# Kernel optimization log

Hardware: AMD Instinct MI355X
Metric: run time of the kernel (lower is better)

Reference implementation:

```python
import jax, jax.numpy as jnp
import numpy as np

B, S, H, D, OUT = 4, 2048, 16, 64, 1024


def setup_inputs() -> dict:
    root = jax.random.key(0)
    ks = jax.random.split(root, 7)
    scale = 0.02
    return {
        "query": jax.random.normal(ks[0], (B, S, D), dtype=jnp.float32),
        "key": jax.random.normal(ks[1], (B, S, D), dtype=jnp.float32),
        "value": jax.random.normal(ks[2], (B, S, D), dtype=jnp.float32),
        # per-head projection weights, torch Linear layout [out, in] stacked over heads
        "Wq": jax.random.normal(ks[3], (H, D, D), dtype=jnp.float32) * scale,
        "Wk": jax.random.normal(ks[4], (H, D, D), dtype=jnp.float32) * scale,
        "Wv": jax.random.normal(ks[5], (H, D, D), dtype=jnp.float32) * scale,
        # output projection weight [output_dim, H*D]
        "Wo": jax.random.normal(ks[6], (OUT, H * D), dtype=jnp.float32) * scale,
    }


def reference(query, key, value, Wq, Wk, Wv, Wo):
    b, s, d = query.shape
    h = Wq.shape[0]
    # per-head linear projections (x @ W_h.T), batched over all heads at once
    q = jnp.einsum('bsd,hed->bhse', query, Wq)   # [B,H,S,D]
    k = jnp.einsum('bsd,hed->bhse', key, Wk)
    v = jnp.einsum('bsd,hed->bhse', value, Wv)
    scores = jnp.einsum('bhqe,bhke->bhqk', q, k) / jnp.sqrt(jnp.asarray(d, q.dtype))
    attn = jax.nn.softmax(scores, axis=-1)       # [B,H,S,S]
    o = jnp.einsum('bhqk,bhke->bhqe', attn, v)   # [B,H,S,D]
    # concat heads along feature dim -> [B,S,H*D]
    x = o.transpose(0, 2, 1, 3).reshape(b, s, h * d)
    return x @ Wo.T                               # [B,S,OUT]
```

## Files before the change

kernel.cpp:

```cpp
#include <hip/hip_runtime.h>
#include <hip/hip_bf16.h>
#include <cstdint>


#define QSCALE 0.1803368801111204f

typedef __attribute__((ext_vector_type(8))) short bf16x8;
typedef __attribute__((ext_vector_type(4))) short bf16x4;
typedef __attribute__((ext_vector_type(4))) float f32x4;
typedef __attribute__((ext_vector_type(16))) float f32x16;

typedef __attribute__((address_space(1))) unsigned int g_u32;
typedef __attribute__((address_space(3))) unsigned int l_u32;

__device__ inline unsigned short f2bf(float f) {
    union { float f; unsigned u; } v;
    v.f = f;
    unsigned r = v.u + 0x7fffu + ((v.u >> 16) & 1u);
    return (unsigned short)(r >> 16);
}

__device__ inline unsigned cvt_pk_bf16(float a, float b) {
    unsigned r;
    asm("v_cvt_pk_bf16_f32 %0, %1, %2" : "=v"(r) : "v"(a), "v"(b));
    return r;
}

__device__ inline f32x4 mfma16(bf16x8 a, bf16x8 b, f32x4 c) {
    return __builtin_amdgcn_mfma_f32_16x16x32_bf16(a, b, c, 0, 0, 0);
}
__device__ inline f32x16 mfma32(bf16x8 a, bf16x8 b, f32x16 c) {
    return __builtin_amdgcn_mfma_f32_32x32x16_bf16(a, b, c, 0, 0, 0);
}

__device__ inline float sum16(const f32x16& v) {
    float a0 = v[0] + v[1], a1 = v[2] + v[3], a2 = v[4] + v[5], a3 = v[6] + v[7];
    float a4 = v[8] + v[9], a5 = v[10] + v[11], a6 = v[12] + v[13], a7 = v[14] + v[15];
    float b0 = a0 + a1, b1 = a2 + a3, b2 = a4 + a5, b3 = a6 + a7;
    return (b0 + b1) + (b2 + b3);
}

__global__ __launch_bounds__(256) void conv_bf16(
    const float* __restrict__ q, const float* __restrict__ k, const float* __restrict__ v,
    const float* __restrict__ wq, const float* __restrict__ wk, const float* __restrict__ wv,
    const float* __restrict__ wo,
    unsigned short* __restrict__ qb, unsigned short* __restrict__ kb,
    unsigned short* __restrict__ vb,
    unsigned short* __restrict__ wqb, unsigned short* __restrict__ wkb,
    unsigned short* __restrict__ wvb, unsigned short* __restrict__ wob) {
    const int z = blockIdx.y;
    const float* src; unsigned short* dst; int n;
    switch (z) {
        case 0: src = q;  dst = qb;  n = 524288;  break;
        case 1: src = k;  dst = kb;  n = 524288;  break;
        case 2: src = v;  dst = vb;  n = 524288;  break;
        case 3: src = wq; dst = wqb; n = 65536;   break;
        case 4: src = wk; dst = wkb; n = 65536;   break;
        case 5: src = wv; dst = wvb; n = 65536;   break;
        default: src = wo; dst = wob; n = 1048576; break;
    }
    int i = (blockIdx.x * 256 + threadIdx.x) * 8;
    if (i >= n) return;
    float4 f0 = *reinterpret_cast<const float4*>(src + i);
    float4 f1 = *reinterpret_cast<const float4*>(src + i + 4);
    bf16x8 h;
    h[0] = (short)f2bf(f0.x); h[1] = (short)f2bf(f0.y);
    h[2] = (short)f2bf(f0.z); h[3] = (short)f2bf(f0.w);
    h[4] = (short)f2bf(f1.x); h[5] = (short)f2bf(f1.y);
    h[6] = (short)f2bf(f1.z); h[7] = (short)f2bf(f1.w);
    *reinterpret_cast<bf16x8*>(dst + i) = h;
}

__global__ __launch_bounds__(256) void qkv_proj(
    const unsigned short* __restrict__ qb, const unsigned short* __restrict__ kb,
    const unsigned short* __restrict__ vb,
    const unsigned short* __restrict__ wqb, const unsigned short* __restrict__ wkb,
    const unsigned short* __restrict__ wvb,
    unsigned short* __restrict__ Qp, unsigned short* __restrict__ Kp,
    unsigned short* __restrict__ Vt) {
    const int z = blockIdx.z;
    const unsigned short* X = (z == 0) ? qb : (z == 1) ? kb : vb;
    const unsigned short* W = (z == 0) ? wqb : (z == 1) ? wkb : wvb;
    const int bh = blockIdx.y;
    const int b = bh >> 4, h = bh & 15;
    const int s0 = blockIdx.x * 64;
    const int t = threadIdx.x;
    const int w = t >> 6, l = t & 63, lr = l & 15, lg = l >> 4;

    __shared__ unsigned short Xs[64][72];
    __shared__ unsigned short Ws[64][72];

    {
        const unsigned short* xsrc = X + (size_t)(b * 2048 + s0) * 64;
        const unsigned short* wsrc = W + h * 4096;
#pragma unroll
        for (int i = 0; i < 2; ++i) {
            int idx = t + i * 256;
            int r = idx >> 3, c8 = (idx & 7) * 8;
            *reinterpret_cast<bf16x8*>(&Xs[r][c8]) =
                *reinterpret_cast<const bf16x8*>(xsrc + (size_t)r * 64 + c8);
            *reinterpret_cast<bf16x8*>(&Ws[r][c8]) =
                *reinterpret_cast<const bf16x8*>(wsrc + r * 64 + c8);
        }
    }
    __syncthreads();

    f32x4 acc[4];
#pragma unroll
    for (int nt = 0; nt < 4; ++nt) acc[nt] = f32x4{0.f, 0.f, 0.f, 0.f};
#pragma unroll
    for (int kk = 0; kk < 2; ++kk) {
        bf16x8 a = *reinterpret_cast<const bf16x8*>(&Xs[w * 16 + lr][kk * 32 + lg * 8]);
#pragma unroll
        for (int nt = 0; nt < 4; ++nt) {
            bf16x8 bb = *reinterpret_cast<const bf16x8*>(&Ws[nt * 16 + lr][kk * 32 + lg * 8]);
            acc[nt] = mfma16(a, bb, acc[nt]);
        }
    }

    const size_t bhS = (size_t)bh * 2048 * 64;
    if (z < 2) {
        unsigned short* Out = (z == 0) ? Qp : Kp;
        const float scale = (z == 0) ? QSCALE : 1.0f;
#pragma unroll
        for (int nt = 0; nt < 4; ++nt)
#pragma unroll
            for (int j = 0; j < 4; ++j) {
                int s = s0 + w * 16 + lg * 4 + j;
                int e = nt * 16 + lr;
                Out[bhS + (size_t)s * 64 + e] = f2bf(acc[nt][j] * scale);
            }
    } else {
#pragma unroll
        for (int nt = 0; nt < 4; ++nt) {
            int e = nt * 16 + lr;
            int s = s0 + w * 16 + lg * 4;
            bf16x4 pk;
#pragma unroll
            for (int j = 0; j < 4; ++j) pk[j] = (short)f2bf(acc[nt][j]);
            *reinterpret_cast<bf16x4*>(&Vt[(size_t)bh * 64 * 2048 + (size_t)e * 2048 + s]) = pk;
        }
    }
}

__global__ __launch_bounds__(256) void attn_kernel(
    const unsigned short* __restrict__ Qp, const unsigned short* __restrict__ Kp,
    const unsigned short* __restrict__ Vt, unsigned short* __restrict__ Xb) {
    const int bh = blockIdx.y;
    const int b = bh >> 4, h = bh & 15;
    const int t = threadIdx.x;
    const int w = t >> 6, l = t & 63;
    const int lo = l & 31, hi = l >> 5;
    const int qw = blockIdx.x * 128 + w * 32;

    __shared__ unsigned short Kbuf[2][4096];
    __shared__ unsigned short Vbuf[2][4096];

    bf16x8 bq[4];
    {
        const unsigned short* qptr = Qp + ((size_t)bh * 2048 + qw + lo) * 64 + hi * 8;
#pragma unroll
        for (int ds = 0; ds < 4; ++ds)
            bq[ds] = *reinterpret_cast<const bf16x8*>(qptr + ds * 16);
    }

    f32x16 oacc0, oacc1;
#pragma unroll
    for (int r = 0; r < 16; ++r) { oacc0[r] = 0.f; oacc1[r] = 0.f; }
    float lsum = 0.f;

    const unsigned short* kbase = Kp + (size_t)bh * 2048 * 64;
    const unsigned short* vbase = Vt + (size_t)bh * 64 * 2048;

    const int rr = l >> 3;
    const int sp = (l & 7) ^ rr;
    const int rb = w * 16;

#pragma unroll
    for (int i = 0; i < 2; ++i) {
        int r = rb + i * 8 + rr;
        __builtin_amdgcn_global_load_lds(
            (const g_u32*)(kbase + (size_t)r * 64 + sp * 8),
            (l_u32*)(&Kbuf[0][(rb + i * 8) * 64]), 16, 0, 0);
        __builtin_amdgcn_global_load_lds(
            (const g_u32*)(vbase + (size_t)r * 2048 + sp * 8),
            (l_u32*)(&Vbuf[0][(rb + i * 8) * 64]), 16, 0, 0);
    }
    __syncthreads();

    for (int kt = 0; kt < 32; ++kt) {
        const int cur = kt & 1;
        if (kt < 31) {
#pragma unroll
            for (int i = 0; i < 2; ++i) {
                int r = rb + i * 8 + rr;
                __builtin_amdgcn_global_load_lds(
                    (const g_u32*)(kbase + (size_t)((kt + 1) * 64 + r) * 64 + sp * 8),
                    (l_u32*)(&Kbuf[cur ^ 1][(rb + i * 8) * 64]), 16, 0, 0);
                __builtin_amdgcn_global_load_lds(
                    (const g_u32*)(vbase + (size_t)r * 2048 + (kt + 1) * 64 + sp * 8),
                    (l_u32*)(&Vbuf[cur ^ 1][(rb + i * 8) * 64]), 16, 0, 0);
            }
        }

        const char* kb = (const char*)Kbuf[cur];
        const char* vb = (const char*)Vbuf[cur];

        f32x16 s0, s1;
#pragma unroll
        for (int r = 0; r < 16; ++r) { s0[r] = 0.f; s1[r] = 0.f; }
        __builtin_amdgcn_s_setprio(1);
#pragma unroll
        for (int ds = 0; ds < 4; ++ds) {
            int c = (32 * ds + 16 * hi) ^ ((lo & 7) << 4);
            bf16x8 ka0 = *reinterpret_cast<const bf16x8*>(kb + lo * 128 + c);
            bf16x8 ka1 = *reinterpret_cast<const bf16x8*>(kb + (lo + 32) * 128 + c);
            s0 = mfma32(ka0, bq[ds], s0);
            s1 = mfma32(ka1, bq[ds], s1);
        }
        __builtin_amdgcn_s_setprio(0);

#pragma unroll
        for (int r = 0; r < 16; ++r) s0[r] = __builtin_amdgcn_exp2f(s0[r]);
#pragma unroll
        for (int r = 0; r < 16; ++r) s1[r] = __builtin_amdgcn_exp2f(s1[r]);
        lsum += sum16(s0) + sum16(s1);

        __builtin_amdgcn_s_setprio(1);
#pragma unroll
        for (int ks = 0; ks < 4; ++ks) {
            f32x16 S = (ks < 2) ? s0 : s1;
            const int bb = (ks & 1) * 8;
            unsigned w0 = cvt_pk_bf16(S[bb + 0], S[bb + 1]);
            unsigned w1 = cvt_pk_bf16(S[bb + 2], S[bb + 3]);
            unsigned w2 = cvt_pk_bf16(S[bb + 4], S[bb + 5]);
            unsigned w3 = cvt_pk_bf16(S[bb + 6], S[bb + 7]);
            asm("v_permlane32_swap_b32 %0, %1" : "+v"(w0), "+v"(w2));
            asm("v_permlane32_swap_b32 %0, %1" : "+v"(w1), "+v"(w3));
            union { unsigned u[4]; bf16x8 v; } pa;
            pa.u[0] = w0; pa.u[1] = w1; pa.u[2] = w2; pa.u[3] = w3;
            int c = (32 * ks + 16 * hi) ^ ((lo & 7) << 4);
            bf16x8 v0 = *reinterpret_cast<const bf16x8*>(vb + lo * 128 + c);
            bf16x8 v1 = *reinterpret_cast<const bf16x8*>(vb + (lo + 32) * 128 + c);
            oacc0 = mfma32(pa.v, v0, oacc0);
            oacc1 = mfma32(pa.v, v1, oacc1);
        }
        __builtin_amdgcn_s_setprio(0);
        __syncthreads();
    }

    lsum += __shfl_xor(lsum, 32);
    const size_t rowbase = (size_t)b * 2048 * 1024 + (size_t)h * 64;
#pragma unroll
    for (int r = 0; r < 16; ++r) {
        int ql = (r & 3) + 8 * (r >> 2) + 4 * hi;
        float inv = 1.0f / __shfl(lsum, ql);
        unsigned short* dst = Xb + rowbase + (size_t)(qw + ql) * 1024;
        dst[lo] = f2bf(oacc0[r] * inv);
        dst[lo + 32] = f2bf(oacc1[r] * inv);
    }
}

__global__ __launch_bounds__(256) void out_gemm(
    const unsigned short* __restrict__ Xb, const unsigned short* __restrict__ Wob,
    float* __restrict__ out) {
    const int nb = blockIdx.x * 128;
    const int mb = blockIdx.y * 128;
    const int t = threadIdx.x;
    const int w = t >> 6, l = t & 63, lr = l & 15, lg = l >> 4;
    const int wr = (w >> 1) * 64, wc = (w & 1) * 64;

    __shared__ unsigned short As[128 * 64];
    __shared__ unsigned short Bs[128 * 64];

    f32x4 acc[4][4];
#pragma unroll
    for (int mi = 0; mi < 4; ++mi)
#pragma unroll
        for (int ni = 0; ni < 4; ++ni) acc[mi][ni] = f32x4{0.f, 0.f, 0.f, 0.f};

    const int rr = l >> 3, p8 = (l & 7) * 8;

    for (int kt = 0; kt < 16; ++kt) {
        __syncthreads();
#pragma unroll
        for (int i = 0; i < 4; ++i) {
            int r = w * 32 + i * 8 + rr;
            __builtin_amdgcn_global_load_lds(
                (const g_u32*)(Xb + (size_t)(mb + r) * 1024 + kt * 64 + p8),
                (l_u32*)(&As[(w * 32 + i * 8) * 64]), 16, 0, 0);
            __builtin_amdgcn_global_load_lds(
                (const g_u32*)(Wob + (size_t)(nb + r) * 1024 + kt * 64 + p8),
                (l_u32*)(&Bs[(w * 32 + i * 8) * 64]), 16, 0, 0);
        }
        __syncthreads();

#pragma unroll
        for (int kk = 0; kk < 2; ++kk) {
            bf16x8 af[4], bf[4];
#pragma unroll
            for (int mi = 0; mi < 4; ++mi)
                af[mi] = *reinterpret_cast<const bf16x8*>(&As[(wr + mi * 16 + lr) * 64 + kk * 32 + lg * 8]);
#pragma unroll
            for (int ni = 0; ni < 4; ++ni)
                bf[ni] = *reinterpret_cast<const bf16x8*>(&Bs[(wc + ni * 16 + lr) * 64 + kk * 32 + lg * 8]);
#pragma unroll
            for (int mi = 0; mi < 4; ++mi)
#pragma unroll
                for (int ni = 0; ni < 4; ++ni)
                    acc[mi][ni] = mfma16(af[mi], bf[ni], acc[mi][ni]);
        }
    }

#pragma unroll
    for (int mi = 0; mi < 4; ++mi)
#pragma unroll
        for (int ni = 0; ni < 4; ++ni)
#pragma unroll
            for (int j = 0; j < 4; ++j)
                out[(size_t)(mb + wr + mi * 16 + lg * 4 + j) * 1024 + nb + wc + ni * 16 + lr] =
                    acc[mi][ni][j];
}

extern "C" void kernel_launch(void* const* d_in, const int* in_sizes, int n_in,
                              void* d_out, int out_size, void* d_ws, size_t ws_size,
                              hipStream_t stream) {
    (void)in_sizes; (void)n_in; (void)out_size; (void)ws_size;
    const float* query = (const float*)d_in[0];
    const float* key   = (const float*)d_in[1];
    const float* value = (const float*)d_in[2];
    const float* Wq = (const float*)d_in[3];
    const float* Wk = (const float*)d_in[4];
    const float* Wv = (const float*)d_in[5];
    const float* Wo = (const float*)d_in[6];
    float* out = (float*)d_out;

    char* ws = (char*)d_ws;
    unsigned short* Qp  = (unsigned short*)(ws);
    unsigned short* Kp  = (unsigned short*)(ws + (size_t)16 * 1024 * 1024);
    unsigned short* Vt  = (unsigned short*)(ws + (size_t)32 * 1024 * 1024);
    unsigned short* Xb  = (unsigned short*)(ws + (size_t)48 * 1024 * 1024);
    unsigned short* qb  = Xb;
    unsigned short* kb  = (unsigned short*)(ws + (size_t)49 * 1024 * 1024);
    unsigned short* vb  = (unsigned short*)(ws + (size_t)50 * 1024 * 1024);
    unsigned short* Wob = (unsigned short*)(ws + (size_t)64 * 1024 * 1024);
    unsigned short* Wqb = (unsigned short*)(ws + (size_t)66 * 1024 * 1024);
    unsigned short* Wkb = Wqb + 65536;
    unsigned short* Wvb = Wkb + 65536;

    hipLaunchKernelGGL(conv_bf16, dim3(512, 7), dim3(256), 0, stream,
                       query, key, value, Wq, Wk, Wv, Wo,
                       qb, kb, vb, Wqb, Wkb, Wvb, Wob);
    hipLaunchKernelGGL(qkv_proj, dim3(32, 64, 3), dim3(256), 0, stream,
                       qb, kb, vb, Wqb, Wkb, Wvb, Qp, Kp, Vt);
    hipLaunchKernelGGL(attn_kernel, dim3(16, 64), dim3(256), 0, stream,
                       Qp, Kp, Vt, Xb);
    hipLaunchKernelGGL(out_gemm, dim3(8, 64), dim3(256), 0, stream,
                       Xb, Wob, out);
}
```

Baseline: 218.1 us.

## Double-buffer output GEMM, swizzle LDS, vectorize stores, and split attention S tiles

The output GEMM now double-buffers its LDS tiles with async global-to-LDS prefetch and XOR-swizzled layout to avoid bank conflicts. Swapping the MFMA operands lets it write float4 rows instead of scalar stores. The Q/K projection also swaps operands so it can emit packed bf16x4 stores. The attention kernel processes its two 32-key halves sequentially to cut register pressure and sets launch bounds for three blocks per CU. The trade-off is more LDS in the GEMM and less independent MFMA work in flight per attention iteration.

```diff
diff --git a/kernel.cpp b/kernel.cpp
--- a/kernel.cpp
+++ b/kernel.cpp
@@ -108,29 +108,38 @@
     f32x4 acc[4];
 #pragma unroll
     for (int nt = 0; nt < 4; ++nt) acc[nt] = f32x4{0.f, 0.f, 0.f, 0.f};
-#pragma unroll
-    for (int kk = 0; kk < 2; ++kk) {
-        bf16x8 a = *reinterpret_cast<const bf16x8*>(&Xs[w * 16 + lr][kk * 32 + lg * 8]);
-#pragma unroll
-        for (int nt = 0; nt < 4; ++nt) {
-            bf16x8 bb = *reinterpret_cast<const bf16x8*>(&Ws[nt * 16 + lr][kk * 32 + lg * 8]);
-            acc[nt] = mfma16(a, bb, acc[nt]);
-        }
-    }
 
     const size_t bhS = (size_t)bh * 2048 * 64;
     if (z < 2) {
+#pragma unroll
+        for (int kk = 0; kk < 2; ++kk) {
+            bf16x8 a = *reinterpret_cast<const bf16x8*>(&Xs[w * 16 + lr][kk * 32 + lg * 8]);
+#pragma unroll
+            for (int nt = 0; nt < 4; ++nt) {
+                bf16x8 bb = *reinterpret_cast<const bf16x8*>(&Ws[nt * 16 + lr][kk * 32 + lg * 8]);
+                acc[nt] = mfma16(bb, a, acc[nt]);
+            }
+        }
         unsigned short* Out = (z == 0) ? Qp : Kp;
         const float scale = (z == 0) ? QSCALE : 1.0f;
-#pragma unroll
-        for (int nt = 0; nt < 4; ++nt)
-#pragma unroll
-            for (int j = 0; j < 4; ++j) {
-                int s = s0 + w * 16 + lg * 4 + j;
-                int e = nt * 16 + lr;
-                Out[bhS + (size_t)s * 64 + e] = f2bf(acc[nt][j] * scale);
-            }
+        const int s = s0 + w * 16 + lr;
+#pragma unroll
+        for (int nt = 0; nt < 4; ++nt) {
+            bf16x4 pk;
+#pragma unroll
+            for (int j = 0; j < 4; ++j) pk[j] = (short)f2bf(acc[nt][j] * scale);
+            *reinterpret_cast<bf16x4*>(&Out[bhS + (size_t)s * 64 + nt * 16 + lg * 4]) = pk;
+        }
     } else {
+#pragma unroll
+        for (int kk = 0; kk < 2; ++kk) {
+            bf16x8 a = *reinterpret_cast<const bf16x8*>(&Xs[w * 16 + lr][kk * 32 + lg * 8]);
+#pragma unroll
+            for (int nt = 0; nt < 4; ++nt) {
+                bf16x8 bb = *reinterpret_cast<const bf16x8*>(&Ws[nt * 16 + lr][kk * 32 + lg * 8]);
+                acc[nt] = mfma16(a, bb, acc[nt]);
+            }
+        }
 #pragma unroll
         for (int nt = 0; nt < 4; ++nt) {
             int e = nt * 16 + lr;
@@ -143,7 +152,7 @@
     }
 }
 
-__global__ __launch_bounds__(256) void attn_kernel(
+__global__ __launch_bounds__(256, 3) void attn_kernel(
     const unsigned short* __restrict__ Qp, const unsigned short* __restrict__ Kp,
     const unsigned short* __restrict__ Vt, unsigned short* __restrict__ Xb) {
     const int bh = blockIdx.y;
@@ -188,6 +197,8 @@
     }
     __syncthreads();
 
+    const int swz = (lo & 7) << 4;
+
     for (int kt = 0; kt < 32; ++kt) {
         const int cur = kt & 1;
         if (kt < 31) {
@@ -206,46 +217,44 @@
         const char* kb = (const char*)Kbuf[cur];
         const char* vb = (const char*)Vbuf[cur];
 
-        f32x16 s0, s1;
-#pragma unroll
-        for (int r = 0; r < 16; ++r) { s0[r] = 0.f; s1[r] = 0.f; }
-        __builtin_amdgcn_s_setprio(1);
-#pragma unroll
-        for (int ds = 0; ds < 4; ++ds) {
-            int c = (32 * ds + 16 * hi) ^ ((lo & 7) << 4);
-            bf16x8 ka0 = *reinterpret_cast<const bf16x8*>(kb + lo * 128 + c);
-            bf16x8 ka1 = *reinterpret_cast<const bf16x8*>(kb + (lo + 32) * 128 + c);
-            s0 = mfma32(ka0, bq[ds], s0);
-            s1 = mfma32(ka1, bq[ds], s1);
-        }
-        __builtin_amdgcn_s_setprio(0);
-
-#pragma unroll
-        for (int r = 0; r < 16; ++r) s0[r] = __builtin_amdgcn_exp2f(s0[r]);
-#pragma unroll
-        for (int r = 0; r < 16; ++r) s1[r] = __builtin_amdgcn_exp2f(s1[r]);
-        lsum += sum16(s0) + sum16(s1);
-
-        __builtin_amdgcn_s_setprio(1);
-#pragma unroll
-        for (int ks = 0; ks < 4; ++ks) {
-            f32x16 S = (ks < 2) ? s0 : s1;
-            const int bb = (ks & 1) * 8;
-            unsigned w0 = cvt_pk_bf16(S[bb + 0], S[bb + 1]);
-            unsigned w1 = cvt_pk_bf16(S[bb + 2], S[bb + 3]);
-            unsigned w2 = cvt_pk_bf16(S[bb + 4], S[bb + 5]);
-            unsigned w3 = cvt_pk_bf16(S[bb + 6], S[bb + 7]);
-            asm("v_permlane32_swap_b32 %0, %1" : "+v"(w0), "+v"(w2));
-            asm("v_permlane32_swap_b32 %0, %1" : "+v"(w1), "+v"(w3));
-            union { unsigned u[4]; bf16x8 v; } pa;
-            pa.u[0] = w0; pa.u[1] = w1; pa.u[2] = w2; pa.u[3] = w3;
-            int c = (32 * ks + 16 * hi) ^ ((lo & 7) << 4);
-            bf16x8 v0 = *reinterpret_cast<const bf16x8*>(vb + lo * 128 + c);
-            bf16x8 v1 = *reinterpret_cast<const bf16x8*>(vb + (lo + 32) * 128 + c);
-            oacc0 = mfma32(pa.v, v0, oacc0);
-            oacc1 = mfma32(pa.v, v1, oacc1);
-        }
-        __builtin_amdgcn_s_setprio(0);
+#pragma unroll
+        for (int half = 0; half < 2; ++half) {
+            f32x16 s;
+#pragma unroll
+            for (int r = 0; r < 16; ++r) s[r] = 0.f;
+            const char* krow = kb + (lo + 32 * half) * 128;
+            __builtin_amdgcn_s_setprio(1);
+#pragma unroll
+            for (int ds = 0; ds < 4; ++ds) {
+                bf16x8 ka = *reinterpret_cast<const bf16x8*>(krow + ((32 * ds + 16 * hi) ^ swz));
+                s = mfma32(ka, bq[ds], s);
+            }
+            __builtin_amdgcn_s_setprio(0);
+
+#pragma unroll
+            for (int r = 0; r < 16; ++r) s[r] = __builtin_amdgcn_exp2f(s[r]);
+            lsum += sum16(s);
+
+#pragma unroll
+            for (int ks2 = 0; ks2 < 2; ++ks2) {
+                const int bb = ks2 * 8;
+                unsigned w0 = cvt_pk_bf16(s[bb + 0], s[bb + 1]);
+                unsigned w1 = cvt_pk_bf16(s[bb + 2], s[bb + 3]);
+                unsigned w2 = cvt_pk_bf16(s[bb + 4], s[bb + 5]);
+                unsigned w3 = cvt_pk_bf16(s[bb + 6], s[bb + 7]);
+                asm("v_permlane32_swap_b32 %0, %1" : "+v"(w0), "+v"(w2));
+                asm("v_permlane32_swap_b32 %0, %1" : "+v"(w1), "+v"(w3));
+                union { unsigned u[4]; bf16x8 v; } pa;
+                pa.u[0] = w0; pa.u[1] = w1; pa.u[2] = w2; pa.u[3] = w3;
+                int c = (32 * (half * 2 + ks2) + 16 * hi) ^ swz;
+                bf16x8 v0 = *reinterpret_cast<const bf16x8*>(vb + lo * 128 + c);
+                bf16x8 v1 = *reinterpret_cast<const bf16x8*>(vb + (lo + 32) * 128 + c);
+                __builtin_amdgcn_s_setprio(1);
+                oacc0 = mfma32(pa.v, v0, oacc0);
+                oacc1 = mfma32(pa.v, v1, oacc1);
+                __builtin_amdgcn_s_setprio(0);
+            }
+        }
         __syncthreads();
     }
 
@@ -270,8 +279,8 @@
     const int w = t >> 6, l = t & 63, lr = l & 15, lg = l >> 4;
     const int wr = (w >> 1) * 64, wc = (w & 1) * 64;
 
-    __shared__ unsigned short As[128 * 64];
-    __shared__ unsigned short Bs[128 * 64];
+    __shared__ unsigned short As[2][128 * 64];
+    __shared__ unsigned short Bs[2][128 * 64];
 
     f32x4 acc[4][4];
 #pragma unroll
@@ -279,47 +288,71 @@
 #pragma unroll
         for (int ni = 0; ni < 4; ++ni) acc[mi][ni] = f32x4{0.f, 0.f, 0.f, 0.f};
 
-    const int rr = l >> 3, p8 = (l & 7) * 8;
+    const int rr = l >> 3;
+    const int sp = (l & 7) ^ rr;
+    const int swz = (lr & 7) << 4;
+
+#pragma unroll
+    for (int i = 0; i < 4; ++i) {
+        int r = w * 32 + i * 8 + rr;
+        __builtin_amdgcn_global_load_lds(
+            (const g_u32*)(Xb + (size_t)(mb + r) * 1024 + sp * 8),
+            (l_u32*)(&As[0][(w * 32 + i * 8) * 64]), 16, 0, 0);
+        __builtin_amdgcn_global_load_lds(
+            (const g_u32*)(Wob + (size_t)(nb + r) * 1024 + sp * 8),
+            (l_u32*)(&Bs[0][(w * 32 + i * 8) * 64]), 16, 0, 0);
+    }
+    __syncthreads();
 
     for (int kt = 0; kt < 16; ++kt) {
+        const int cur = kt & 1;
+        if (kt < 15) {
+#pragma unroll
+            for (int i = 0; i < 4; ++i) {
+                int r = w * 32 + i * 8 + rr;
+                __builtin_amdgcn_global_load_lds(
+                    (const g_u32*)(Xb + (size_t)(mb + r) * 1024 + (kt + 1) * 64 + sp * 8),
+                    (l_u32*)(&As[cur ^ 1][(w * 32 + i * 8) * 64]), 16, 0, 0);
+                __builtin_amdgcn_global_load_lds(
+                    (const g_u32*)(Wob + (size_t)(nb + r) * 1024 + (kt + 1) * 64 + sp * 8),
+                    (l_u32*)(&Bs[cur ^ 1][(w * 32 + i * 8) * 64]), 16, 0, 0);
+            }
+        }
+
+        const char* ab = (const char*)As[cur];
+        const char* bbp = (const char*)Bs[cur];
+#pragma unroll
+        for (int kk = 0; kk < 2; ++kk) {
+            const int cb = (kk * 64 + lg * 16) ^ swz;
+            bf16x8 af[4], bf[4];
+#pragma unroll
+            for (int mi = 0; mi < 4; ++mi)
+                af[mi] = *reinterpret_cast<const bf16x8*>(ab + (wr + mi * 16 + lr) * 128 + cb);
+#pragma unroll
+            for (int ni = 0; ni < 4; ++ni)
+                bf[ni] = *reinterpret_cast<const bf16x8*>(bbp + (wc + ni * 16 + lr) * 128 + cb);
+            __builtin_amdgcn_s_setprio(1);
+#pragma unroll
+            for (int mi = 0; mi < 4; ++mi)
+#pragma unroll
+                for (int ni = 0; ni < 4; ++ni)
+                    acc[mi][ni] = mfma16(bf[ni], af[mi], acc[mi][ni]);
+            __builtin_amdgcn_s_setprio(0);
+        }
         __syncthreads();
-#pragma unroll
-        for (int i = 0; i < 4; ++i) {
-            int r = w * 32 + i * 8 + rr;
-            __builtin_amdgcn_global_load_lds(
-                (const g_u32*)(Xb + (size_t)(mb + r) * 1024 + kt * 64 + p8),
-                (l_u32*)(&As[(w * 32 + i * 8) * 64]), 16, 0, 0);
-            __builtin_amdgcn_global_load_lds(
-                (const g_u32*)(Wob + (size_t)(nb + r) * 1024 + kt * 64 + p8),
-                (l_u32*)(&Bs[(w * 32 + i * 8) * 64]), 16, 0, 0);
-        }
-        __syncthreads();
-
-#pragma unroll
-        for (int kk = 0; kk < 2; ++kk) {
-            bf16x8 af[4], bf[4];
-#pragma unroll
-            for (int mi = 0; mi < 4; ++mi)
-                af[mi] = *reinterpret_cast<const bf16x8*>(&As[(wr + mi * 16 + lr) * 64 + kk * 32 + lg * 8]);
-#pragma unroll
-            for (int ni = 0; ni < 4; ++ni)
-                bf[ni] = *reinterpret_cast<const bf16x8*>(&Bs[(wc + ni * 16 + lr) * 64 + kk * 32 + lg * 8]);
-#pragma unroll
-            for (int mi = 0; mi < 4; ++mi)
-#pragma unroll
-                for (int ni = 0; ni < 4; ++ni)
-                    acc[mi][ni] = mfma16(af[mi], bf[ni], acc[mi][ni]);
-        }
-    }
-
-#pragma unroll
-    for (int mi = 0; mi < 4; ++mi)
-#pragma unroll
-        for (int ni = 0; ni < 4; ++ni)
-#pragma unroll
-            for (int j = 0; j < 4; ++j)
-                out[(size_t)(mb + wr + mi * 16 + lg * 4 + j) * 1024 + nb + wc + ni * 16 + lr] =
-                    acc[mi][ni][j];
+    }
+
+#pragma unroll
+    for (int mi = 0; mi < 4; ++mi) {
+        const size_t row = (size_t)(mb + wr + mi * 16 + lr);
+#pragma unroll
+        for (int ni = 0; ni < 4; ++ni) {
+            float4 o;
+            o.x = acc[mi][ni][0]; o.y = acc[mi][ni][1];
+            o.z = acc[mi][ni][2]; o.w = acc[mi][ni][3];
+            *reinterpret_cast<float4*>(&out[row * 1024 + nb + wc + ni * 16 + lg * 4]) = o;
+        }
+    }
 }
 
 extern "C" void kernel_launch(void* const* d_in, const int* in_sizes, int n_in,
```

After: 203.4 us. 6.7% less time.
